# Kernel tuning notes

Hardware: AMD Instinct MI355X
Metric: run time of the kernel (lower is better)

## Reference

```python
import jax, jax.numpy as jnp
import numpy as np

B, NQ, NKV, QD, KVD, AD = 8, 4096, 4096, 1024, 1024, 128

def setup_inputs() -> dict:
    key = jax.random.key(0)
    ks = jax.random.split(key, 6)
    scale = lambda d: 1.0 / np.sqrt(d)
    return {
        "q": jax.random.normal(ks[0], (B, NQ, QD), dtype=jnp.float32),
        "k": jax.random.normal(ks[1], (B, NKV, KVD), dtype=jnp.float32),
        "v": jax.random.normal(ks[2], (B, NKV, KVD), dtype=jnp.float32),
        "Wq": jax.random.normal(ks[3], (QD, AD), dtype=jnp.float32) * scale(QD),
        "Wk": jax.random.normal(ks[4], (KVD, AD), dtype=jnp.float32) * scale(KVD),
        "Wv": jax.random.normal(ks[5], (KVD, AD), dtype=jnp.float32) * scale(KVD),
    }

def reference(q, k, v, Wq, Wk, Wv):
    s = AD ** (-0.5)
    Q = jnp.einsum('bnd,de->bne', q, Wq)   # [B,NQ,AD]
    K = jnp.einsum('bmd,de->bme', k, Wk)   # [B,NKV,AD]
    V = jnp.einsum('bmd,de->bme', v, Wv)   # [B,NKV,AD]
    sc = jnp.einsum('bne,bme->bnm', Q, K) * s  # [B,NQ,NKV]
    att = jax.nn.softmax(sc, axis=-1)
    return jnp.einsum('bnm,bme->bne', att, V)
```

## Files before the change

kernel.cpp:

```cpp
#include <hip/hip_runtime.h>
#include <cstdint>
#include <cstddef>

typedef __bf16 bf16_t;
typedef __bf16 bf16x8 __attribute__((ext_vector_type(8)));
typedef __bf16 bf16x4v __attribute__((ext_vector_type(4)));
typedef float f32x16 __attribute__((ext_vector_type(16)));

static __device__ __forceinline__ f32x16 mfma32(bf16x8 a, bf16x8 b, f32x16 c) {
  return __builtin_amdgcn_mfma_f32_32x32x16_bf16(a, b, c, 0, 0, 0);
}

static __device__ __forceinline__ void gld_lds16(const void* g, void* l) {
  __builtin_amdgcn_global_load_lds(
      (const __attribute__((address_space(1))) unsigned int*)g,
      (__attribute__((address_space(3))) unsigned int*)l, 16, 0, 0);
}

#define CEXP_CONST 0.12754582f


__global__ void wt_kernel(const float* __restrict__ Wq, const float* __restrict__ Wk,
                          const float* __restrict__ Wv, bf16_t* __restrict__ Wt2) {
  int t = blockIdx.x * 256 + threadIdx.x;
  int tensor = t >> 17;
  int r = t & 131071;
  int j = r & 7, l31 = (r >> 3) & 31, h = (r >> 8) & 1, nf = (r >> 9) & 3, k16 = (r >> 11) & 63;
  int k = k16 * 16 + h * 8 + j, n = nf * 32 + l31;
  const float* W = tensor == 0 ? Wq : (tensor == 1 ? Wk : Wv);
  Wt2[t] = (bf16_t)W[(size_t)k * 128 + n];
}

__global__ __launch_bounds__(256, 2) void proj_kernel(
    const float* __restrict__ xq, const float* __restrict__ xk, const float* __restrict__ xv,
    const bf16_t* __restrict__ WtAll,
    bf16_t* __restrict__ Qp, bf16_t* __restrict__ Kp, bf16_t* __restrict__ Vt) {
  __shared__ __align__(16) char smc[65536];
  const int tid = threadIdx.x;
  const int ty = blockIdx.y;
  const int bm = blockIdx.x;
  const float* X = (ty == 0) ? xq : (ty == 1) ? xk : xv;
  const bf16_t* W2 = WtAll + (size_t)ty * 131072;
  const int lane = tid & 63;
  const int w = tid >> 6;
  const int l31 = lane & 31, h = lane >> 5;

  const char* aG = (const char*)X + (size_t)bm * 131072;

  float4 gA[8], gB[8];
  auto ldg = [&](float4 (&buf)[8], int g) {
#pragma unroll
    for (int i = 0; i < 8; ++i)
      buf[i] = *(const float4*)(aG + (size_t)((g * 2048 + i * 256 + tid) << 4));
  };
  auto stg = [&](float4 (&buf)[8], int g) {
#pragma unroll
    for (int i = 0; i < 8; ++i) {
      int c = g * 2048 + i * 256 + tid;
      int row = c >> 8, slot = c & 255;
      bf16x4v bv;
      bv[0] = (bf16_t)buf[i].x; bv[1] = (bf16_t)buf[i].y;
      bv[2] = (bf16_t)buf[i].z; bv[3] = (bf16_t)buf[i].w;
      int dst = row * 2048 + (((slot >> 1) ^ (row & 7)) << 4) + (slot & 1) * 8;
      *(uint2*)(smc + dst) = __builtin_bit_cast(uint2, bv);
    }
  };

  ldg(gA, 0);
  ldg(gB, 1);
  stg(gA, 0);
  ldg(gA, 2);
  stg(gB, 1);
  ldg(gB, 3);
  stg(gA, 2);
  stg(gB, 3);
  __syncthreads();

  f32x16 acc;
#pragma unroll
  for (int r = 0; r < 16; ++r) acc[r] = 0.0f;
  const bf16_t* wbase = W2 + w * 512 + lane * 8;
  const char* arow = smc + l31 * 2048;
  const int asw = l31 & 7;
#pragma unroll 16
  for (int k16 = 0; k16 < 64; ++k16) {
    bf16x8 af = *(const bf16x8*)(arow + ((((k16 << 1) | h) ^ asw) << 4));
    bf16x8 wf = *(const bf16x8*)(wbase + (size_t)k16 * 2048);
    acc = mfma32(af, wf, acc);
  }
  __syncthreads();

  if (ty < 2) {
    constexpr int RS = 264;
#pragma unroll
    for (int r = 0; r < 16; ++r) {
      int m = (r & 3) + 8 * (r >> 2) + 4 * h;
      *(bf16_t*)(smc + m * RS + (w * 32 + l31) * 2) = (bf16_t)acc[r];
    }
    __syncthreads();
    bf16_t* O = (ty == 0) ? Qp : Kp;
    char* obase = (char*)O + (size_t)bm * 8192;
#pragma unroll
    for (int i = 0; i < 2; ++i) {
      int c = i * 256 + tid;
      int rr = c >> 4, ch = c & 15;
      uint4 vv = *(const uint4*)(smc + rr * RS + ch * 16);
      *(uint4*)(obase + rr * 256 + ch * 16) = vv;
    }
  } else {
#pragma unroll
    for (int q = 0; q < 4; ++q) {
      int n = w * 32 + l31;
      bf16x4v bv;
#pragma unroll
      for (int j = 0; j < 4; ++j) bv[j] = (bf16_t)acc[q * 4 + j];
      *(uint2*)(smc + n * 72 + q * 16 + h * 8) = __builtin_bit_cast(uint2, bv);
    }
    __syncthreads();
    const int bb = bm >> 7;
    const int m0 = (bm & 127) * 32;
    {
      int n = tid >> 1, half = tid & 1;
      const char* src = smc + n * 72 + half * 32;
      char* dst = (char*)Vt + (size_t)bb * 1048576 + (size_t)n * 8192 + m0 * 2 + half * 32;
      uint4 v0 = *(const uint4*)(src);
      uint4 v1 = *(const uint4*)(src + 16);
      *(uint4*)(dst) = v0;
      *(uint4*)(dst + 16) = v1;
    }
  }
}

template <int B0>
static __device__ __forceinline__ bf16x8 build_pf(const f32x16& s, int h) {
  unsigned c0, c1, c2, c3;
  asm("v_cvt_pk_bf16_f32 %0, %1, %2" : "=v"(c0) : "v"(s[B0 + 0]), "v"(s[B0 + 1]));
  asm("v_cvt_pk_bf16_f32 %0, %1, %2" : "=v"(c1) : "v"(s[B0 + 2]), "v"(s[B0 + 3]));
  asm("v_cvt_pk_bf16_f32 %0, %1, %2" : "=v"(c2) : "v"(s[B0 + 4]), "v"(s[B0 + 5]));
  asm("v_cvt_pk_bf16_f32 %0, %1, %2" : "=v"(c3) : "v"(s[B0 + 6]), "v"(s[B0 + 7]));
  unsigned x0 = (unsigned)__shfl_xor((int)c0, 32);
  unsigned x1 = (unsigned)__shfl_xor((int)c1, 32);
  unsigned x2 = (unsigned)__shfl_xor((int)c2, 32);
  unsigned x3 = (unsigned)__shfl_xor((int)c3, 32);
  uint4 u;
  u.x = h ? x2 : c0;
  u.y = h ? x3 : c1;
  u.z = h ? c2 : x0;
  u.w = h ? c3 : x1;
  return __builtin_bit_cast(bf16x8, u);
}

template <int SPLIT>
__global__ __launch_bounds__(256, 2) void attn_kernel(
    const bf16_t* __restrict__ Qp, const bf16_t* __restrict__ Kp,
    const bf16_t* __restrict__ Vt, float* __restrict__ out,
    float* __restrict__ Opart, float* __restrict__ Mpart, float* __restrict__ Lpart) {
  __shared__ __align__(16) char smc[65536];
  const int tid = threadIdx.x;
  const int lane = tid & 63, w = tid >> 6;
  const int l31 = lane & 31, h = lane >> 5;
  const int bid = blockIdx.x;
  const int b = bid & 7;
  const int qt = (bid >> 3) & 31;
  const int s = bid >> 8;
  const int NT = 64 / SPLIT;
  const float CEXP = CEXP_CONST;
  const int qbase = qt * 128 + w * 32;
  const int sw0 = (l31 ^ (l31 >> 3)) & 7;
  const int sw1 = sw0 ^ 4;

  bf16x8 qf[8];
  const bf16_t* qrow = Qp + (size_t)(b * 4096 + qbase + l31) * 128 + h * 8;
#pragma unroll
  for (int db = 0; db < 8; ++db) qf[db] = *(const bf16x8*)(qrow + db * 16);

  int swv[4];
#pragma unroll
  for (int nf = 0; nf < 4; ++nf) swv[nf] = (l31 & 7) ^ ((4 * nf + (l31 >> 3)) & 7);

  const int rl = lane >> 4, slK = lane & 15;
  const int dl = lane >> 3, slV = lane & 7;
  int koff[4], voff[4];
#pragma unroll
  for (int i = 0; i < 4; ++i) {
    int r = w * 16 + i * 4 + rl;
    int swr = (r ^ (r >> 3)) & 7;
    koff[i] = r * 256 + (((slK & 8) | ((slK & 7) ^ swr)) << 4);
    int d = w * 32 + i * 8 + dl;
    int swd = (d ^ (d >> 3)) & 7;
    voff[i] = d * 8192 + ((slV ^ swd) << 4);
  }
  const char* kpb = (const char*)Kp + (size_t)b * 1048576 + (size_t)s * NT * 16384;
  const char* vpb = (const char*)Vt + (size_t)b * 1048576 + (size_t)s * NT * 128;

  f32x16 oacc[4];
#pragma unroll
  for (int nf = 0; nf < 4; ++nf)
#pragma unroll
    for (int r = 0; r < 16; ++r) oacc[nf][r] = 0.0f;
  float m_run = -3.0e38f, lacc = 0.0f;

  auto stage = [&](int tt, int bufb) {
    const char* kb = kpb + (size_t)tt * 16384;
    const char* vb = vpb + (size_t)tt * 128;
    char* lk = smc + bufb + w * 4096;
    char* lv = smc + bufb + 16384 + w * 4096;
#pragma unroll
    for (int i = 0; i < 4; ++i) {
      gld_lds16(kb + koff[i], lk + i * 1024);
      gld_lds16(vb + voff[i], lv + i * 1024);
    }
  };

  stage(0, 0);
  stage(1, 32768);

  for (int t = 0; t < NT; ++t) {
    asm volatile("s_waitcnt vmcnt(8)" ::: "memory");
    __builtin_amdgcn_s_barrier();
    const char* kb = smc + (t & 1) * 32768;
    const char* vb = kb + 16384;

    f32x16 s0, s1;
#pragma unroll
    for (int i = 0; i < 16; ++i) { s0[i] = 0.0f; s1[i] = 0.0f; }
    __builtin_amdgcn_s_setprio(1);
#pragma unroll
    for (int db = 0; db < 8; ++db) {
      const int q = 2 * db + h;
      bf16x8 k0 = *(const bf16x8*)(kb + l31 * 256 + (((q & 8) | ((q & 7) ^ sw0)) << 4));
      bf16x8 k1 = *(const bf16x8*)(kb + (32 + l31) * 256 + (((q & 8) | ((q & 7) ^ sw1)) << 4));
      s0 = mfma32(k0, qf[db], s0);
      s1 = mfma32(k1, qf[db], s1);
    }
    __builtin_amdgcn_s_setprio(0);

    float tmax = fmaxf(s0[0], s1[0]);
#pragma unroll
    for (int i = 1; i < 16; ++i) tmax = fmaxf(tmax, fmaxf(s0[i], s1[i]));
    tmax = fmaxf(tmax, __shfl_xor(tmax, 32));
    if (__any(tmax > m_run + 62.0f)) {
      float mnew = fmaxf(m_run, tmax);
      float fac = exp2f((m_run - mnew) * CEXP);
      m_run = mnew;
      lacc *= fac;
#pragma unroll
      for (int r = 0; r < 16; ++r) {
        float fr = __shfl(fac, (r & 3) + 8 * (r >> 2) + 4 * h);
#pragma unroll
        for (int nf = 0; nf < 4; ++nf) oacc[nf][r] *= fr;
      }
    }
    const float mc = m_run * CEXP;
#pragma unroll
    for (int i = 0; i < 16; ++i) s0[i] = exp2f(fmaf(s0[i], CEXP, -mc));
#pragma unroll
    for (int i = 0; i < 16; ++i) s1[i] = exp2f(fmaf(s1[i], CEXP, -mc));
    float a0 = 0.f, a1 = 0.f, a2 = 0.f, a3 = 0.f;
#pragma unroll
    for (int i = 0; i < 16; i += 4) {
      a0 += s0[i] + s1[i];         a1 += s0[i + 1] + s1[i + 1];
      a2 += s0[i + 2] + s1[i + 2]; a3 += s0[i + 3] + s1[i + 3];
    }
    lacc += (a0 + a1) + (a2 + a3);

    __builtin_amdgcn_s_setprio(1);
    {
      bf16x8 pf = build_pf<0>(s0, h);
#pragma unroll
      for (int nf = 0; nf < 4; ++nf) {
        bf16x8 vf = *(const bf16x8*)(vb + (nf * 32 + l31) * 128 + (((0 + h) ^ swv[nf]) << 4));
        oacc[nf] = mfma32(pf, vf, oacc[nf]);
      }
    }
    {
      bf16x8 pf = build_pf<8>(s0, h);
#pragma unroll
      for (int nf = 0; nf < 4; ++nf) {
        bf16x8 vf = *(const bf16x8*)(vb + (nf * 32 + l31) * 128 + (((2 + h) ^ swv[nf]) << 4));
        oacc[nf] = mfma32(pf, vf, oacc[nf]);
      }
    }
    {
      bf16x8 pf = build_pf<0>(s1, h);
#pragma unroll
      for (int nf = 0; nf < 4; ++nf) {
        bf16x8 vf = *(const bf16x8*)(vb + (nf * 32 + l31) * 128 + (((4 + h) ^ swv[nf]) << 4));
        oacc[nf] = mfma32(pf, vf, oacc[nf]);
      }
    }
    {
      bf16x8 pf = build_pf<8>(s1, h);
#pragma unroll
      for (int nf = 0; nf < 4; ++nf) {
        bf16x8 vf = *(const bf16x8*)(vb + (nf * 32 + l31) * 128 + (((6 + h) ^ swv[nf]) << 4));
        oacc[nf] = mfma32(pf, vf, oacc[nf]);
      }
    }
    __builtin_amdgcn_s_setprio(0);

    __builtin_amdgcn_s_barrier();
    stage((t + 2) & (NT - 1), (t & 1) * 32768);
  }
  asm volatile("s_waitcnt vmcnt(0)" ::: "memory");

  lacc += __shfl_xor(lacc, 32);
  if (SPLIT == 1) {
    const float inv = 1.0f / lacc;
    float* ob = out + (size_t)(b * 4096 + qbase) * 128;
#pragma unroll
    for (int r = 0; r < 16; ++r) {
      const int rowD = (r & 3) + 8 * (r >> 2) + 4 * h;
      float ir = __shfl(inv, rowD);
#pragma unroll
      for (int nf = 0; nf < 4; ++nf)
        ob[(size_t)rowD * 128 + nf * 32 + l31] = oacc[nf][r] * ir;
    }
  } else {
    const int pb = s * 256 + b * 32 + qt;
    if (lane < 32) {
      Mpart[pb * 128 + w * 32 + l31] = m_run;
      Lpart[pb * 128 + w * 32 + l31] = lacc;
    }
    float* ob = Opart + ((size_t)pb * 128 + w * 32) * 128;
#pragma unroll
    for (int r = 0; r < 16; ++r) {
      const int rowD = (r & 3) + 8 * (r >> 2) + 4 * h;
#pragma unroll
      for (int nf = 0; nf < 4; ++nf)
        ob[(size_t)rowD * 128 + nf * 32 + l31] = oacc[nf][r];
    }
  }
}

__global__ __launch_bounds__(256) void combine_kernel(
    const float* __restrict__ Opart, const float* __restrict__ Mpart,
    const float* __restrict__ Lpart, float* __restrict__ out) {
  const int g = blockIdx.x * 8 + (threadIdx.x >> 5);
  const int lane32 = threadIdx.x & 31;
  const int b = g >> 12;
  const int pos = g & 4095;
  const int qt = pos >> 7;
  const int row = pos & 127;
  const int i0 = (b * 32 + qt) * 128 + row;
  const int i1 = (256 + b * 32 + qt) * 128 + row;
  const float m0 = Mpart[i0], m1 = Mpart[i1];
  const float l0 = Lpart[i0], l1 = Lpart[i1];
  const float m = fmaxf(m0, m1);
  const float w0 = exp2f((m0 - m) * CEXP_CONST);
  const float w1 = exp2f((m1 - m) * CEXP_CONST);
  const float inv = 1.0f / (w0 * l0 + w1 * l1);
  const float4 o0 = *(const float4*)(Opart + (size_t)i0 * 128 + lane32 * 4);
  const float4 o1 = *(const float4*)(Opart + (size_t)i1 * 128 + lane32 * 4);
  float4 o;
  o.x = (w0 * o0.x + w1 * o1.x) * inv;
  o.y = (w0 * o0.y + w1 * o1.y) * inv;
  o.z = (w0 * o0.z + w1 * o1.z) * inv;
  o.w = (w0 * o0.w + w1 * o1.w) * inv;
  *(float4*)(out + (size_t)g * 128 + lane32 * 4) = o;
}

extern "C" void kernel_launch(void* const* d_in, const int* in_sizes, int n_in,
                              void* d_out, int out_size, void* d_ws, size_t ws_size,
                              hipStream_t stream) {
  const float* q  = (const float*)d_in[0];
  const float* k  = (const float*)d_in[1];
  const float* v  = (const float*)d_in[2];
  const float* Wq = (const float*)d_in[3];
  const float* Wk = (const float*)d_in[4];
  const float* Wv = (const float*)d_in[5];
  float* out = (float*)d_out;
  char* ws = (char*)d_ws;
  bf16_t* Wt2 = (bf16_t*)(ws);
  bf16_t* Qp = (bf16_t*)(ws + (size_t)(1u << 20));
  bf16_t* Kp = (bf16_t*)(ws + (size_t)(9u << 20));
  bf16_t* Vt = (bf16_t*)(ws + (size_t)(17u << 20));
  float* Opart = (float*)(ws + (size_t)(32u << 20));
  float* Mpart = (float*)(ws + (size_t)(64u << 20));
  float* Lpart = (float*)(ws + (size_t)(64u << 20) + (256u << 10));

  hipLaunchKernelGGL(wt_kernel, dim3(1536), dim3(256), 0, stream, Wq, Wk, Wv, Wt2);
  hipLaunchKernelGGL(proj_kernel, dim3(1024, 3), dim3(256), 0, stream, q, k, v, Wt2, Qp, Kp, Vt);

  if (ws_size >= ((size_t)65 << 20)) {
    hipLaunchKernelGGL((attn_kernel<2>), dim3(512), dim3(256), 0, stream,
                       Qp, Kp, Vt, out, Opart, Mpart, Lpart);
    hipLaunchKernelGGL(combine_kernel, dim3(4096), dim3(256), 0, stream,
                       Opart, Mpart, Lpart, out);
  } else {
    hipLaunchKernelGGL((attn_kernel<1>), dim3(256), dim3(256), 0, stream,
                       Qp, Kp, Vt, out, Opart, Mpart, Lpart);
  }
}
```

Before: 214.0 us.

## Pipeline projection K-loop with double-buffered LDS and smaller shared memory

The projection kernel used to load the whole 32x1024 activation tile into 64KB of LDS before computing. It now streams the tile in eight K-chunks through two 8KB LDS buffers, with register prefetch, so global loads overlap the MFMA loop. The LDS footprint drops to 16KB and launch bounds rise to 4 blocks per CU to raise occupancy. The cost is extra barriers per chunk and tighter register pressure under the higher occupancy bound.

```diff
diff --git a/kernel.cpp b/kernel.cpp
--- a/kernel.cpp
+++ b/kernel.cpp
@@ -31,11 +31,11 @@
   Wt2[t] = (bf16_t)W[(size_t)k * 128 + n];
 }
 
-__global__ __launch_bounds__(256, 2) void proj_kernel(
+__global__ __launch_bounds__(256, 4) void proj_kernel(
     const float* __restrict__ xq, const float* __restrict__ xk, const float* __restrict__ xv,
     const bf16_t* __restrict__ WtAll,
     bf16_t* __restrict__ Qp, bf16_t* __restrict__ Kp, bf16_t* __restrict__ Vt) {
-  __shared__ __align__(16) char smc[65536];
+  __shared__ __align__(16) char smc[16384];
   const int tid = threadIdx.x;
   const int ty = blockIdx.y;
   const int bm = blockIdx.x;
@@ -47,46 +47,73 @@
 
   const char* aG = (const char*)X + (size_t)bm * 131072;
 
-  float4 gA[8], gB[8];
-  auto ldg = [&](float4 (&buf)[8], int g) {
-#pragma unroll
-    for (int i = 0; i < 8; ++i)
-      buf[i] = *(const float4*)(aG + (size_t)((g * 2048 + i * 256 + tid) << 4));
+  float4 S0[4], S1[4];
+  auto ldg = [&](float4 (&S)[4], int p) {
+#pragma unroll
+    for (int i = 0; i < 4; ++i) {
+      int c = i * 256 + tid;
+      S[i] = *(const float4*)(aG + (size_t)(c >> 5) * 4096 + p * 512 + (c & 31) * 16);
+    }
   };
-  auto stg = [&](float4 (&buf)[8], int g) {
-#pragma unroll
-    for (int i = 0; i < 8; ++i) {
-      int c = g * 2048 + i * 256 + tid;
-      int row = c >> 8, slot = c & 255;
+  auto stg = [&](float4 (&S)[4], int buf) {
+#pragma unroll
+    for (int i = 0; i < 4; ++i) {
+      int c = i * 256 + tid;
+      int row = c >> 5, s = c & 31;
       bf16x4v bv;
-      bv[0] = (bf16_t)buf[i].x; bv[1] = (bf16_t)buf[i].y;
-      bv[2] = (bf16_t)buf[i].z; bv[3] = (bf16_t)buf[i].w;
-      int dst = row * 2048 + (((slot >> 1) ^ (row & 7)) << 4) + (slot & 1) * 8;
+      bv[0] = (bf16_t)S[i].x; bv[1] = (bf16_t)S[i].y;
+      bv[2] = (bf16_t)S[i].z; bv[3] = (bf16_t)S[i].w;
+      int dst = buf * 8192 + row * 256 + ((((s >> 1) ^ (row & 7)) << 4)) + (s & 1) * 8;
       *(uint2*)(smc + dst) = __builtin_bit_cast(uint2, bv);
     }
   };
-
-  ldg(gA, 0);
-  ldg(gB, 1);
-  stg(gA, 0);
-  ldg(gA, 2);
-  stg(gB, 1);
-  ldg(gB, 3);
-  stg(gA, 2);
-  stg(gB, 3);
-  __syncthreads();
 
   f32x16 acc;
 #pragma unroll
   for (int r = 0; r < 16; ++r) acc[r] = 0.0f;
   const bf16_t* wbase = W2 + w * 512 + lane * 8;
-  const char* arow = smc + l31 * 2048;
   const int asw = l31 & 7;
-#pragma unroll 16
-  for (int k16 = 0; k16 < 64; ++k16) {
-    bf16x8 af = *(const bf16x8*)(arow + ((((k16 << 1) | h) ^ asw) << 4));
-    bf16x8 wf = *(const bf16x8*)(wbase + (size_t)k16 * 2048);
-    acc = mfma32(af, wf, acc);
+  const char* arow0 = smc + l31 * 256;
+
+  auto kloop = [&](int p) {
+    const char* arow = arow0 + (p & 1) * 8192;
+    const bf16_t* wp = wbase + (size_t)(p * 8) * 2048;
+#pragma unroll
+    for (int kk = 0; kk < 8; ++kk) {
+      bf16x8 af = *(const bf16x8*)(arow + (((kk * 2 + h) ^ asw) << 4));
+      bf16x8 wf = *(const bf16x8*)(wp + (size_t)kk * 2048);
+      acc = mfma32(af, wf, acc);
+    }
+  };
+
+  ldg(S0, 0);
+  ldg(S1, 1);
+  stg(S0, 0);
+  ldg(S0, 2);
+  __syncthreads();
+
+#pragma unroll
+  for (int p2 = 0; p2 < 4; ++p2) {
+    {
+      const int p = 2 * p2;
+      kloop(p);
+      __builtin_amdgcn_s_barrier();
+      stg(S1, 1);
+      if (p + 3 < 8) ldg(S1, p + 3);
+      asm volatile("s_waitcnt lgkmcnt(0)" ::: "memory");
+      __builtin_amdgcn_s_barrier();
+    }
+    {
+      const int p = 2 * p2 + 1;
+      kloop(p);
+      __builtin_amdgcn_s_barrier();
+      if (p < 7) {
+        stg(S0, 0);
+        if (p + 3 < 8) ldg(S0, p + 3);
+        asm volatile("s_waitcnt lgkmcnt(0)" ::: "memory");
+      }
+      __builtin_amdgcn_s_barrier();
+    }
   }
   __syncthreads();
 
```

After: 209.9 us. Within noise of the previous version (-1.9%).
